# Kernel optimization log

Hardware: AMD Instinct MI355X
Metric: run time of the kernel (lower is better)

## Reference

```python
import jax, jax.numpy as jnp
import numpy as np

TAU = 18.0


def smooth_compose(X, M, tau=TAU):
    # Z[n,i,j] = smooth_min(X[n,i], M[i,j]) = -(1/tau) * log(exp(-tau*X) + exp(-tau*M))
    # Y[n,j]   = (1/tau) * logsumexp(tau * Z[n,:,j], axis over i)
    # tau*Z = -logaddexp(-tau*X, -tau*M)  (numerically stable, same math)
    tZ = -jnp.logaddexp(-tau * X[:, :, None], -tau * M[None, :, :])  # [n, d, d]
    return (1.0 / tau) * jax.nn.logsumexp(tZ, axis=1)  # [n, d]


def setup_inputs() -> dict:
    key = jax.random.key(0)
    k1, k2, k3, k4, k5 = jax.random.split(key, 5)
    n, p, d = 2048, 1024, 256
    S = jax.random.uniform(k1, (n, p), dtype=jnp.float32)
    T = jax.random.uniform(k2, (n, p), dtype=jnp.float32)
    # learned parameters (A0/M0/B0 defaults are 0.5-filled; use random values of similar scale)
    A = jax.random.uniform(k3, (p, d), dtype=jnp.float32)
    # rawM = logit(M0); random small logits -> M = sigmoid(rawM) near 0.5
    rawM = 0.5 * jax.random.normal(k4, (d, d), dtype=jnp.float32)
    B = jax.random.uniform(k5, (d, p), dtype=jnp.float32)
    return {"S": S, "T": T, "A": A, "rawM": rawM, "B": B}


def reference(S, T, A, rawM, B):
    M = jax.nn.sigmoid(rawM)            # [d, d]
    X_hat = S @ A                       # [n, d]
    Y_hat = T @ A                       # [n, d]
    X_box = jnp.clip(X_hat, 0.0, 1.0)
    Y_box = jnp.clip(Y_hat, 0.0, 1.0)
    Y_pred = smooth_compose(X_box, M, tau=TAU)  # [n, d]
    S_rec = X_hat @ B                   # [n, p]
    T_rec = Y_hat @ B                   # [n, p]
    T_pred = Y_pred @ B                 # [n, p]
    return (X_hat, Y_hat, X_box, Y_box, Y_pred, S_rec, T_rec, T_pred)
```

## Files before the change

### kernel.cpp

```cpp
#include <hip/hip_runtime.h>
#include <math.h>

constexpr int N = 2048;
constexpr int P = 1024;
constexpr int D = 256;
constexpr float TAU = 18.0f;

constexpr size_t OFF_XHAT  = 0;
constexpr size_t OFF_YHAT  = (size_t)N * D;
constexpr size_t OFF_XBOX  = 2 * (size_t)N * D;
constexpr size_t OFF_YBOX  = 3 * (size_t)N * D;
constexpr size_t OFF_YPRED = 4 * (size_t)N * D;
constexpr size_t OFF_SREC  = 5 * (size_t)N * D;

constexpr size_t WS_ATH = 0;
constexpr size_t WS_ATL = 524288;
constexpr size_t WS_BTH = 1048576;
constexpr size_t WS_BTL = 1572864;
constexpr size_t WS_V   = 2097152;
constexpr size_t WS_U   = 2359296;
constexpr size_t WS_LHH = 4456448;
constexpr size_t WS_LHL = 7602176;
constexpr size_t WS_STH = 10747904;
constexpr size_t WS_STL = 19136512;
constexpr size_t WS_MIN = 27525120;

typedef short bhalf8 __attribute__((ext_vector_type(8)));
typedef float f32x4  __attribute__((ext_vector_type(4)));

__device__ inline short f2bf(float f) {
  union { float f; unsigned u; } x; x.f = f;
  unsigned r = (x.u + 0x7FFFu + ((x.u >> 16) & 1u)) >> 16;
  return (short)r;
}
__device__ inline float bf2f(short h) {
  union { unsigned u; float f; } x; x.u = ((unsigned)(unsigned short)h) << 16;
  return x.f;
}
__device__ inline int xcd_swz(int bid, int nwg) {
  const int cpx = nwg >> 3;
  return (bid & 7) * cpx + (bid >> 3);
}

__device__ inline void transpose_hilo_body(
    const float* __restrict__ src, short* __restrict__ dh,
    short* __restrict__ dl, int R, int C, int bx, int by, int t) {
  __shared__ __align__(16) float tile[32][36];
  const int r0 = bx * 32, c0 = by * 32;
  {
    const int tr = t >> 3, tc4 = (t & 7) * 4;
    float4 x = *(const float4*)(src + (size_t)(r0 + tr) * C + c0 + tc4);
    *(float4*)&tile[tr][tc4] = x;
  }
  __syncthreads();
  {
    const int tc = t >> 3, tr4 = (t & 7) * 4;
    short4 h, l;
    float f0 = tile[tr4 + 0][tc];
    float f1 = tile[tr4 + 1][tc];
    float f2 = tile[tr4 + 2][tc];
    float f3 = tile[tr4 + 3][tc];
    h.x = f2bf(f0); l.x = f2bf(f0 - bf2f(h.x));
    h.y = f2bf(f1); l.y = f2bf(f1 - bf2f(h.y));
    h.z = f2bf(f2); l.z = f2bf(f2 - bf2f(h.z));
    h.w = f2bf(f3); l.w = f2bf(f3 - bf2f(h.w));
    *(short4*)(dh + (size_t)(c0 + tc) * R + r0 + tr4) = h;
    *(short4*)(dl + (size_t)(c0 + tc) * R + r0 + tr4) = l;
  }
}

__global__ __launch_bounds__(256) void prep_all_kernel(
    const float* __restrict__ S, const float* __restrict__ Tm,
    const float* __restrict__ A, const float* __restrict__ rawM,
    const float* __restrict__ B, short* __restrict__ Ath,
    short* __restrict__ Atl, short* __restrict__ Bth,
    short* __restrict__ Btl, float* __restrict__ V,
    short* __restrict__ STh, short* __restrict__ STl,
    int* __restrict__ minx) {
  const int bid = blockIdx.x;
  const int t = threadIdx.x;
  if (bid < 64) {
    if (bid == 0 && t == 0) *minx = 0x7F800000;
    const int idx = (bid * 256 + t) * 4;
    float4 x = *(const float4*)(rawM + idx);
    float4 o;
    o.x = expf(-TAU / (1.0f + expf(-x.x)));
    o.y = expf(-TAU / (1.0f + expf(-x.y)));
    o.z = expf(-TAU / (1.0f + expf(-x.z)));
    o.w = expf(-TAU / (1.0f + expf(-x.w)));
    *(float4*)(V + idx) = o;
  } else if (bid < 320) {
    const int idx = bid - 64;
    transpose_hilo_body(A, Ath, Atl, P, D, idx & 31, idx >> 5, t);
  } else if (bid < 576) {
    const int idx = bid - 320;
    transpose_hilo_body(B, Bth, Btl, D, P, idx & 7, idx >> 3, t);
  } else {
    const int idx = bid - 576;
#pragma unroll
    for (int q = 0; q < 4; ++q) {
      const int row = idx * 4 + q;
      const float* src = (row < N) ? (S + (size_t)row * P)
                                   : (Tm + (size_t)(row - N) * P);
      float4 x = *(const float4*)(src + t * 4);
      short4 h, l;
      h.x = f2bf(x.x); l.x = f2bf(x.x - bf2f(h.x));
      h.y = f2bf(x.y); l.y = f2bf(x.y - bf2f(h.y));
      h.z = f2bf(x.z); l.z = f2bf(x.z - bf2f(h.z));
      h.w = f2bf(x.w); l.w = f2bf(x.w - bf2f(h.w));
      *(short4*)(STh + (size_t)row * P + t * 4) = h;
      *(short4*)(STl + (size_t)row * P + t * 4) = l;
    }
  }
}

__global__ __launch_bounds__(256) void gemm1_mfma(
    const short* __restrict__ STh, const short* __restrict__ STl,
    const short* __restrict__ Ath, const short* __restrict__ Atl,
    float* __restrict__ out, float* __restrict__ U,
    short* __restrict__ LHh, short* __restrict__ LHl,
    int* __restrict__ minx) {
  __shared__ __align__(16) short As_h[2][32][72];
  __shared__ __align__(16) short As_l[2][32][72];
  __shared__ __align__(16) short Bs_h[2][64][72];
  __shared__ __align__(16) short Bs_l[2][64][72];

  const int t  = threadIdx.x;
  const int wg = xcd_swz(blockIdx.x, 512);
  const int m0 = (wg >> 2) * 32, n0 = (wg & 3) * 64;

  const int arow = t >> 3;
  const int ak   = (t & 7) * 8;
  const short* AhR = STh + (size_t)(m0 + arow) * P;
  const short* AlR = STl + (size_t)(m0 + arow) * P;
  const int brow = t >> 2;
  const int bk   = (t & 3) * 16;
  const short* BhR = Ath + (size_t)(n0 + brow) * P;
  const short* BlR = Atl + (size_t)(n0 + brow) * P;

  const int l = t & 63, w = t >> 6;
  const int wr = (w & 1) * 16, wc = (w >> 1) * 32;
  const int fr = l & 15, ko8 = (l >> 4) * 8, rq = (l >> 4) * 4;

  f32x4 acc[2];
  acc[0] = (f32x4){0.f, 0.f, 0.f, 0.f};
  acc[1] = (f32x4){0.f, 0.f, 0.f, 0.f};

  bhalf8 pah, pal, pbh0, pbh1, pbl0, pbl1;
  pah  = *(const bhalf8*)(AhR + ak);
  pal  = *(const bhalf8*)(AlR + ak);
  pbh0 = *(const bhalf8*)(BhR + bk);
  pbh1 = *(const bhalf8*)(BhR + bk + 8);
  pbl0 = *(const bhalf8*)(BlR + bk);
  pbl1 = *(const bhalf8*)(BlR + bk + 8);

#define STAGE1(buf)                                   \
  do {                                                \
    *(bhalf8*)&As_h[buf][arow][ak]    = pah;          \
    *(bhalf8*)&As_l[buf][arow][ak]    = pal;          \
    *(bhalf8*)&Bs_h[buf][brow][bk]    = pbh0;         \
    *(bhalf8*)&Bs_h[buf][brow][bk+8]  = pbh1;         \
    *(bhalf8*)&Bs_l[buf][brow][bk]    = pbl0;         \
    *(bhalf8*)&Bs_l[buf][brow][bk+8]  = pbl1;         \
  } while (0)

  STAGE1(0);

  for (int ks = 0; ks < 16; ++ks) {
    const int b = ks & 1;
    if (ks < 15) {
      const int kn = (ks + 1) * 64;
      pah  = *(const bhalf8*)(AhR + kn + ak);
      pal  = *(const bhalf8*)(AlR + kn + ak);
      pbh0 = *(const bhalf8*)(BhR + kn + bk);
      pbh1 = *(const bhalf8*)(BhR + kn + bk + 8);
      pbl0 = *(const bhalf8*)(BlR + kn + bk);
      pbl1 = *(const bhalf8*)(BlR + kn + bk + 8);
    }
    __syncthreads();
#pragma unroll
    for (int ks2 = 0; ks2 < 2; ++ks2) {
      const int ko = ks2 * 32 + ko8;
      bhalf8 ahv = *(const bhalf8*)&As_h[b][wr + fr][ko];
      bhalf8 alv = *(const bhalf8*)&As_l[b][wr + fr][ko];
#pragma unroll
      for (int ni = 0; ni < 2; ++ni) {
        bhalf8 bhv = *(const bhalf8*)&Bs_h[b][wc + ni * 16 + fr][ko];
        bhalf8 blv = *(const bhalf8*)&Bs_l[b][wc + ni * 16 + fr][ko];
        acc[ni] = __builtin_amdgcn_mfma_f32_16x16x32_bf16(ahv, bhv, acc[ni], 0, 0, 0);
        acc[ni] = __builtin_amdgcn_mfma_f32_16x16x32_bf16(ahv, blv, acc[ni], 0, 0, 0);
        acc[ni] = __builtin_amdgcn_mfma_f32_16x16x32_bf16(alv, bhv, acc[ni], 0, 0, 0);
      }
    }
    if (ks < 15) STAGE1((ks + 1) & 1);
  }
#undef STAGE1

  float lmin = 3.0e38f;
#pragma unroll
  for (int ni = 0; ni < 2; ++ni) {
    const int col = n0 + wc + ni * 16 + fr;
#pragma unroll
    for (int r = 0; r < 4; ++r) {
      const int row = m0 + wr + rq + r;
      const float v = acc[ni][r];
      const float c = fminf(fmaxf(v, 0.0f), 1.0f);
      const short h  = f2bf(v);
      const short lo = f2bf(v - bf2f(h));
      lmin = fminf(lmin, v);
      LHh[(size_t)row * D + col] = h;
      LHl[(size_t)row * D + col] = lo;
      if (row < N) {
        out[OFF_XHAT + (size_t)row * D + col] = v;
        out[OFF_XBOX + (size_t)row * D + col] = c;
        U[(size_t)row * D + col] = expf(-TAU * c);
      } else {
        const size_t ry = (size_t)(row - N);
        out[OFF_YHAT + ry * D + col] = v;
        out[OFF_YBOX + ry * D + col] = c;
      }
    }
  }
  if (m0 < N) {
#pragma unroll
    for (int off = 32; off; off >>= 1) lmin = fminf(lmin, __shfl_xor(lmin, off));
    if (l == 0) atomicMin(minx, __float_as_int(lmin));
  }
}

__global__ __launch_bounds__(256) void smooth_kernel(
    const float* __restrict__ U, const float* __restrict__ V,
    float* __restrict__ ypred, short* __restrict__ LHh,
    short* __restrict__ LHl, const float* __restrict__ minx) {
  if (*minx >= 1.0f) return;
  __shared__ float us[256][34];
  const int t = threadIdx.x;
  const int n0 = blockIdx.x * 32, j0 = blockIdx.y * 32;

  {
    const int sr = t & 31;
    const int si = (t >> 5) * 32;
    const float* up = U + (size_t)(n0 + sr) * D + si;
#pragma unroll
    for (int q = 0; q < 32; q += 4) {
      float4 x = *(const float4*)(up + q);
      us[si + q + 0][sr] = x.x;
      us[si + q + 1][sr] = x.y;
      us[si + q + 2][sr] = x.z;
      us[si + q + 3][sr] = x.w;
    }
  }
  __syncthreads();

  const int jg = (t & 15) * 2;
  const int nn = (t >> 4) * 2;
  const float* vp = V + j0 + jg;

  float acc00 = 0.f, acc01 = 0.f, acc10 = 0.f, acc11 = 0.f;
#pragma unroll 8
  for (int i = 0; i < D; ++i) {
    float2 u2 = *(const float2*)&us[i][nn];
    float2 v2 = *(const float2*)(vp + (size_t)i * D);
    acc00 += __builtin_amdgcn_rcpf(u2.x + v2.x);
    acc01 += __builtin_amdgcn_rcpf(u2.x + v2.y);
    acc10 += __builtin_amdgcn_rcpf(u2.y + v2.x);
    acc11 += __builtin_amdgcn_rcpf(u2.y + v2.y);
  }

  float a[2][2] = {{acc00, acc01}, {acc10, acc11}};
#pragma unroll
  for (int pI = 0; pI < 2; ++pI) {
    const int row = n0 + nn + pI;
    float2 o;
    o.x = (1.0f / TAU) * logf(a[pI][0]);
    o.y = (1.0f / TAU) * logf(a[pI][1]);
    *(float2*)(ypred + (size_t)row * D + j0 + jg) = o;
    short2 h2, l2;
    h2.x = f2bf(o.x); l2.x = f2bf(o.x - bf2f(h2.x));
    h2.y = f2bf(o.y); l2.y = f2bf(o.y - bf2f(h2.y));
    const size_t lrow = (size_t)(2 * N + row) * D + j0 + jg;
    *(short2*)(LHh + lrow) = h2;
    *(short2*)(LHl + lrow) = l2;
  }
}

__global__ __launch_bounds__(256) void smooth_bcast(
    const float* __restrict__ V, const float* __restrict__ minx,
    float* __restrict__ ypred, short* __restrict__ LHh,
    short* __restrict__ LHl) {
  if (!(*minx >= 1.0f)) return;
  const int t = threadIdx.x;
  const float u0 = expf(-TAU);
  float acc = 0.f;
#pragma unroll 8
  for (int i = 0; i < D; ++i)
    acc += __builtin_amdgcn_rcpf(u0 + V[(size_t)i * D + t]);
  const float y = (1.0f / TAU) * logf(acc);
  const short h  = f2bf(y);
  const short lo = f2bf(y - bf2f(h));
  const int r0 = blockIdx.x * 8;
#pragma unroll
  for (int q = 0; q < 8; ++q) {
    const int row = r0 + q;
    ypred[(size_t)row * D + t] = y;
    LHh[(size_t)(2 * N + row) * D + t] = h;
    LHl[(size_t)(2 * N + row) * D + t] = lo;
  }
}

__global__ __launch_bounds__(512) void gemm2_mfma(
    const short* __restrict__ LHh, const short* __restrict__ LHl,
    const short* __restrict__ Bth, const short* __restrict__ Btl,
    float* __restrict__ rec) {
  __shared__ __align__(16) short As_h[2][128][40];
  __shared__ __align__(16) short As_l[2][128][40];
  __shared__ __align__(16) short Bs_h[2][64][40];
  __shared__ __align__(16) short Bs_l[2][64][40];

  const int t  = threadIdx.x;
  const int wg = xcd_swz(blockIdx.x, 768);
  const int m0 = (wg >> 4) * 128, n0 = (wg & 15) * 64;

  const int arow = t >> 2;
  const int ak   = (t & 3) * 8;
  const short* AhR = LHh + (size_t)(m0 + arow) * D;
  const short* AlR = LHl + (size_t)(m0 + arow) * D;
  const int brow = t >> 3;
  const int bk   = (t & 7) * 4;
  const short* BhR = Bth + (size_t)(n0 + brow) * D;
  const short* BlR = Btl + (size_t)(n0 + brow) * D;

  const int l = t & 63, w = t >> 6;
  const int wr = (w & 3) * 32, wc = (w >> 2) * 32;
  const int fr = l & 15, ko8 = (l >> 4) * 8, rq = (l >> 4) * 4;

  f32x4 acc[2][2];
#pragma unroll
  for (int i = 0; i < 2; ++i)
#pragma unroll
    for (int j = 0; j < 2; ++j) acc[i][j] = (f32x4){0.f, 0.f, 0.f, 0.f};

  bhalf8 pah, pal;
  short4 pbh, pbl;
  pah = *(const bhalf8*)(AhR + ak);
  pal = *(const bhalf8*)(AlR + ak);
  pbh = *(const short4*)(BhR + bk);
  pbl = *(const short4*)(BlR + bk);

#define STAGE2(buf)                            \
  do {                                         \
    *(bhalf8*)&As_h[buf][arow][ak] = pah;      \
    *(bhalf8*)&As_l[buf][arow][ak] = pal;      \
    *(short4*)&Bs_h[buf][brow][bk] = pbh;      \
    *(short4*)&Bs_l[buf][brow][bk] = pbl;      \
  } while (0)

  STAGE2(0);

  for (int ks = 0; ks < 8; ++ks) {
    const int b = ks & 1;
    if (ks < 7) {
      const int kn = (ks + 1) * 32;
      pah = *(const bhalf8*)(AhR + kn + ak);
      pal = *(const bhalf8*)(AlR + kn + ak);
      pbh = *(const short4*)(BhR + kn + bk);
      pbl = *(const short4*)(BlR + kn + bk);
    }
    __syncthreads();
    bhalf8 ahv[2], alv[2], bhv[2], blv[2];
#pragma unroll
    for (int mi = 0; mi < 2; ++mi) {
      ahv[mi] = *(const bhalf8*)&As_h[b][wr + mi * 16 + fr][ko8];
      alv[mi] = *(const bhalf8*)&As_l[b][wr + mi * 16 + fr][ko8];
      bhv[mi] = *(const bhalf8*)&Bs_h[b][wc + mi * 16 + fr][ko8];
      blv[mi] = *(const bhalf8*)&Bs_l[b][wc + mi * 16 + fr][ko8];
    }
#pragma unroll
    for (int mi = 0; mi < 2; ++mi)
#pragma unroll
      for (int ni = 0; ni < 2; ++ni) {
        acc[mi][ni] = __builtin_amdgcn_mfma_f32_16x16x32_bf16(ahv[mi], bhv[ni], acc[mi][ni], 0, 0, 0);
        acc[mi][ni] = __builtin_amdgcn_mfma_f32_16x16x32_bf16(ahv[mi], blv[ni], acc[mi][ni], 0, 0, 0);
        acc[mi][ni] = __builtin_amdgcn_mfma_f32_16x16x32_bf16(alv[mi], bhv[ni], acc[mi][ni], 0, 0, 0);
      }
    if (ks < 7) STAGE2((ks + 1) & 1);
  }
#undef STAGE2

#pragma unroll
  for (int mi = 0; mi < 2; ++mi)
#pragma unroll
    for (int ni = 0; ni < 2; ++ni) {
      const int col = n0 + wc + ni * 16 + fr;
#pragma unroll
      for (int r = 0; r < 4; ++r) {
        const int row = m0 + wr + mi * 16 + rq + r;
        rec[(size_t)row * P + col] = acc[mi][ni][r];
      }
    }
}

extern "C" void kernel_launch(void* const* d_in, const int* in_sizes, int n_in,
                              void* d_out, int out_size, void* d_ws,
                              size_t ws_size, hipStream_t stream) {
  const float* S    = (const float*)d_in[0];
  const float* T    = (const float*)d_in[1];
  const float* A    = (const float*)d_in[2];
  const float* rawM = (const float*)d_in[3];
  const float* B    = (const float*)d_in[4];
  float* out = (float*)d_out;
  char* ws = (char*)d_ws;

  short* Ath = (short*)(ws + WS_ATH);
  short* Atl = (short*)(ws + WS_ATL);
  short* Bth = (short*)(ws + WS_BTH);
  short* Btl = (short*)(ws + WS_BTL);
  float* V   = (float*)(ws + WS_V);
  float* U   = (float*)(ws + WS_U);
  short* LHh = (short*)(ws + WS_LHH);
  short* LHl = (short*)(ws + WS_LHL);
  short* STh = (short*)(ws + WS_STH);
  short* STl = (short*)(ws + WS_STL);
  int*   mnx = (int*)(ws + WS_MIN);

  prep_all_kernel<<<1600, 256, 0, stream>>>(S, T, A, rawM, B, Ath, Atl, Bth,
                                            Btl, V, STh, STl, mnx);
  gemm1_mfma<<<512, 256, 0, stream>>>(STh, STl, Ath, Atl, out, U, LHh, LHl,
                                      mnx);
  smooth_kernel<<<dim3(64, 8), 256, 0, stream>>>(U, V, out + OFF_YPRED, LHh,
                                                 LHl, (const float*)mnx);
  smooth_bcast<<<256, 256, 0, stream>>>(V, (const float*)mnx, out + OFF_YPRED,
                                        LHh, LHl);
  gemm2_mfma<<<768, 512, 0, stream>>>(LHh, LHl, Bth, Btl, out + OFF_SREC);
}
```

Before: 134.0 us.

## Compute broadcast T_pred directly in smooth kernel and skip its GEMM tiles

When every clipped X value is saturated (min >= 1), each Y_pred row is the same vector. In that case the smooth kernel now computes that single row times B in fp32 and broadcasts it into T_pred. The gemm2 blocks covering the T_pred rows return early. The two smooth kernels are also merged into one launch that chooses its path at runtime. This drops a third of the second GEMM's MFMA work and one kernel launch. The cost is a small per-block matvec and some redundant LH writes that are no longer read.

After: 154.7 us. 15.4% more time.

```diff
diff --git a/kernel.cpp b/kernel.cpp
--- a/kernel.cpp
+++ b/kernel.cpp
@@ -12,6 +12,7 @@
 constexpr size_t OFF_YBOX  = 3 * (size_t)N * D;
 constexpr size_t OFF_YPRED = 4 * (size_t)N * D;
 constexpr size_t OFF_SREC  = 5 * (size_t)N * D;
+constexpr size_t OFF_TPRED = OFF_SREC + 2 * (size_t)N * P;
 
 constexpr size_t WS_ATH = 0;
 constexpr size_t WS_ATL = 524288;
@@ -228,15 +229,59 @@
   }
 }
 
-__global__ __launch_bounds__(256) void smooth_kernel(
+__global__ __launch_bounds__(256) void smooth_any(
     const float* __restrict__ U, const float* __restrict__ V,
-    float* __restrict__ ypred, short* __restrict__ LHh,
-    short* __restrict__ LHl, const float* __restrict__ minx) {
-  if (*minx >= 1.0f) return;
+    const float* __restrict__ B, float* __restrict__ ypred,
+    short* __restrict__ LHh, short* __restrict__ LHl,
+    float* __restrict__ tpred, const float* __restrict__ minx) {
+  const int bid = blockIdx.x;
+  const int t = threadIdx.x;
+  const bool fast = (*minx >= 1.0f);
+
+  if (fast) {
+    if (bid >= 64) return;
+    __shared__ float ysh[256];
+    const float u0 = expf(-TAU);
+    float acc = 0.f;
+#pragma unroll 8
+    for (int i = 0; i < D; ++i)
+      acc += __builtin_amdgcn_rcpf(u0 + V[(size_t)i * D + t]);
+    const float y = (1.0f / TAU) * logf(acc);
+    ysh[t] = y;
+    const short h  = f2bf(y);
+    const short lo = f2bf(y - bf2f(h));
+    const int r0 = bid * 32;
+#pragma unroll
+    for (int q = 0; q < 32; ++q) {
+      const int row = r0 + q;
+      ypred[(size_t)row * D + t] = y;
+      LHh[(size_t)(2 * N + row) * D + t] = h;
+      LHl[(size_t)(2 * N + row) * D + t] = lo;
+    }
+    __syncthreads();
+    float2 a01 = {0.f, 0.f}, a23 = {0.f, 0.f};
+    const int c0 = 2 * t;
+#pragma unroll 8
+    for (int k = 0; k < D; ++k) {
+      const float yk = ysh[k];
+      float2 b0 = *(const float2*)(B + (size_t)k * P + c0);
+      float2 b1 = *(const float2*)(B + (size_t)k * P + 512 + c0);
+      a01.x = fmaf(yk, b0.x, a01.x);
+      a01.y = fmaf(yk, b0.y, a01.y);
+      a23.x = fmaf(yk, b1.x, a23.x);
+      a23.y = fmaf(yk, b1.y, a23.y);
+    }
+#pragma unroll
+    for (int q = 0; q < 32; ++q) {
+      const size_t base = (size_t)(r0 + q) * P;
+      *(float2*)(tpred + base + c0)       = a01;
+      *(float2*)(tpred + base + 512 + c0) = a23;
+    }
+    return;
+  }
+
   __shared__ float us[256][34];
-  const int t = threadIdx.x;
-  const int n0 = blockIdx.x * 32, j0 = blockIdx.y * 32;
-
+  const int n0 = (bid >> 3) * 32, j0 = (bid & 7) * 32;
   {
     const int sr = t & 31;
     const int si = (t >> 5) * 32;
@@ -284,34 +329,10 @@
   }
 }
 
-__global__ __launch_bounds__(256) void smooth_bcast(
-    const float* __restrict__ V, const float* __restrict__ minx,
-    float* __restrict__ ypred, short* __restrict__ LHh,
-    short* __restrict__ LHl) {
-  if (!(*minx >= 1.0f)) return;
-  const int t = threadIdx.x;
-  const float u0 = expf(-TAU);
-  float acc = 0.f;
-#pragma unroll 8
-  for (int i = 0; i < D; ++i)
-    acc += __builtin_amdgcn_rcpf(u0 + V[(size_t)i * D + t]);
-  const float y = (1.0f / TAU) * logf(acc);
-  const short h  = f2bf(y);
-  const short lo = f2bf(y - bf2f(h));
-  const int r0 = blockIdx.x * 8;
-#pragma unroll
-  for (int q = 0; q < 8; ++q) {
-    const int row = r0 + q;
-    ypred[(size_t)row * D + t] = y;
-    LHh[(size_t)(2 * N + row) * D + t] = h;
-    LHl[(size_t)(2 * N + row) * D + t] = lo;
-  }
-}
-
 __global__ __launch_bounds__(512) void gemm2_mfma(
     const short* __restrict__ LHh, const short* __restrict__ LHl,
     const short* __restrict__ Bth, const short* __restrict__ Btl,
-    float* __restrict__ rec) {
+    float* __restrict__ rec, const float* __restrict__ minx) {
   __shared__ __align__(16) short As_h[2][128][40];
   __shared__ __align__(16) short As_l[2][128][40];
   __shared__ __align__(16) short Bs_h[2][64][40];
@@ -320,6 +341,8 @@
   const int t  = threadIdx.x;
   const int wg = xcd_swz(blockIdx.x, 768);
   const int m0 = (wg >> 4) * 128, n0 = (wg & 15) * 64;
+
+  if (m0 >= 2 * N && *minx >= 1.0f) return;
 
   const int arow = t >> 2;
   const int ak   = (t & 3) * 8;
@@ -427,9 +450,8 @@
                                             Btl, V, STh, STl, mnx);
   gemm1_mfma<<<512, 256, 0, stream>>>(STh, STl, Ath, Atl, out, U, LHh, LHl,
                                       mnx);
-  smooth_kernel<<<dim3(64, 8), 256, 0, stream>>>(U, V, out + OFF_YPRED, LHh,
-                                                 LHl, (const float*)mnx);
-  smooth_bcast<<<256, 256, 0, stream>>>(V, (const float*)mnx, out + OFF_YPRED,
-                                        LHh, LHl);
-  gemm2_mfma<<<768, 512, 0, stream>>>(LHh, LHl, Bth, Btl, out + OFF_SREC);
-}
+  smooth_any<<<512, 256, 0, stream>>>(U, V, B, out + OFF_YPRED, LHh, LHl,
+                                      out + OFF_TPRED, (const float*)mnx);
+  gemm2_mfma<<<768, 512, 0, stream>>>(LHh, LHl, Bth, Btl, out + OFF_SREC,
+                                      (const float*)mnx);
+}
```
